# Performance work log

Hardware: AMD Instinct MI355X
Metric: run time of the kernel (lower is better)

## Reference

```python
import jax, jax.numpy as jnp
import numpy as np

DIM = 1024
NUM_HEADS = 16
SCALE = DIM ** (-0.5)  # NOTE: source scales by full dim, not head_dim


def setup_inputs() -> dict:
    key = jax.random.key(0)
    ks = jax.random.split(key, 10)
    B, N, C = 2, 2048, DIM
    s = 0.02
    return {
        "x": jax.random.normal(ks[0], (B, N, C), dtype=jnp.float32),
        "queries": jax.random.normal(ks[1], (B, N, C), dtype=jnp.float32),
        "wq": jax.random.normal(ks[2], (C, C), dtype=jnp.float32) * s,
        "bq": jnp.zeros((C,), dtype=jnp.float32),
        "wk": jax.random.normal(ks[3], (C, C), dtype=jnp.float32) * s,
        "bk": jnp.zeros((C,), dtype=jnp.float32),
        "wv": jax.random.normal(ks[4], (C, C), dtype=jnp.float32) * s,
        "bv": jnp.zeros((C,), dtype=jnp.float32),
        "wo": jax.random.normal(ks[5], (C, C), dtype=jnp.float32) * s,
        "bo": jnp.zeros((C,), dtype=jnp.float32),
    }


def reference(x, queries, wq, bq, wk, bk, wv, bv, wo, bo):
    B, N, C = queries.shape
    H = NUM_HEADS
    D = C // H
    # torch Linear: y = x @ W.T + b  (W is [out, in])
    q = (queries @ wq.T + bq).reshape(B, N, H, D).transpose(0, 2, 1, 3)  # [B,H,N,D]
    k = (x @ wk.T + bk).reshape(B, N, H, D).transpose(0, 2, 1, 3)
    v = (x @ wv.T + bv).reshape(B, N, H, D).transpose(0, 2, 1, 3)
    attn = jnp.einsum("bhqd,bhkd->bhqk", q, k) * SCALE  # full-dim scale per source
    attn = jax.nn.softmax(attn, axis=-1)
    out = jnp.einsum("bhqk,bhkd->bhqd", attn, v)  # [B,H,N,D]
    out = out.transpose(0, 2, 1, 3).reshape(B, N, C)
    return out @ wo.T + bo
```

## Files before the change

### kernel.cpp

```cpp
#include <hip/hip_runtime.h>
#include <hip/hip_bf16.h>

typedef __attribute__((ext_vector_type(8))) short bf16x8;
typedef __attribute__((ext_vector_type(4))) float f32x4;
typedef unsigned short u16;
typedef unsigned int u32;

#define MFMA16(a,b,c) __builtin_amdgcn_mfma_f32_16x16x32_bf16((a),(b),(c),0,0,0)

#if defined(__has_builtin) && __has_builtin(__builtin_amdgcn_exp2f)
#define EXP2(x) __builtin_amdgcn_exp2f(x)
#else
#define EXP2(x) exp2f(x)
#endif

#define QSCALE 0.045084220027780106f

__device__ __forceinline__ u16 f2bf(float f) {
  union { float f; unsigned int u; } v; v.f = f;
  unsigned int r = v.u + 0x7FFFu + ((v.u >> 16) & 1u);
  return (u16)(r >> 16);
}

__device__ __forceinline__ u32 pkbf(float a, float b) {
  union { __hip_bfloat162 h; u32 u; } cv;
  cv.h = __float22bfloat162_rn(make_float2(a, b));
  return cv.u;
}

__device__ __forceinline__ void gld16(const void* g, void* l) {
  __builtin_amdgcn_global_load_lds(
      (__attribute__((address_space(1))) void*)(g),
      (__attribute__((address_space(3))) void*)(l), 16, 0, 0);
}

__global__ __launch_bounds__(256) void cast_all(
    const float* __restrict__ x, const float* __restrict__ qu,
    const float* __restrict__ wq, const float* __restrict__ wk,
    const float* __restrict__ wv, const float* __restrict__ wo,
    u16* __restrict__ xb, u16* __restrict__ qub,
    u16* __restrict__ wqb, u16* __restrict__ wkb,
    u16* __restrict__ wvb, u16* __restrict__ wob)
{
  int i = blockIdx.x * 256 + threadIdx.x;
  const float4* src; u16* dst; int off;
  if (i < 1048576)      { src = (const float4*)qu; dst = qub; off = i; }
  else if (i < 2097152) { src = (const float4*)x;  dst = xb;  off = i - 1048576; }
  else if (i < 2359296) { src = (const float4*)wq; dst = wqb; off = i - 2097152; }
  else if (i < 2621440) { src = (const float4*)wk; dst = wkb; off = i - 2359296; }
  else if (i < 2883584) { src = (const float4*)wv; dst = wvb; off = i - 2621440; }
  else                  { src = (const float4*)wo; dst = wob; off = i - 2883584; }
  float4 v = src[off];
  ushort4 r; r.x = f2bf(v.x); r.y = f2bf(v.y); r.z = f2bf(v.z); r.w = f2bf(v.w);
  ((ushort4*)dst)[off] = r;
}

__global__ __launch_bounds__(256) void gemm_qkv(
    const u16* __restrict__ qub, const u16* __restrict__ xb,
    const u16* __restrict__ wqb, const u16* __restrict__ wkb, const u16* __restrict__ wvb,
    const float* __restrict__ bq, const float* __restrict__ bk, const float* __restrict__ bv,
    u16* __restrict__ qhd, u16* __restrict__ khd, u16* __restrict__ vtd)
{
  __shared__ u16 As[128 * 64];
  __shared__ u16 Bs[128 * 64];
  int tid = threadIdx.x, w = tid >> 6, lane = tid & 63;
  int c = lane & 15, quad = lane >> 4;
  int bm = blockIdx.x, bn = blockIdx.y, z = blockIdx.z;
  int wm = w >> 1, wn = w & 1;
  const u16* A = (z == 0) ? qub : xb;
  const u16* W = (z == 0) ? wqb : (z == 1) ? wkb : wvb;
  f32x4 acc[4][4] = {};
  for (int k0 = 0; k0 < 1024; k0 += 64) {
#pragma unroll
    for (int i = 0; i < 4; i++) {
      int seg = i * 256 + w * 64 + lane;
      int row = seg >> 3, pseg = seg & 7;
      int lseg = pseg ^ (row & 7);
      gld16(A + (size_t)(bm * 128 + row) * 1024 + k0 + lseg * 8,
            &As[(i * 256 + w * 64) * 8]);
      gld16(W + (size_t)(bn * 128 + row) * 1024 + k0 + lseg * 8,
            &Bs[(i * 256 + w * 64) * 8]);
    }
    __syncthreads();
#pragma unroll
    for (int ks = 0; ks < 2; ks++) {
      bf16x8 af[4], bfr[4];
#pragma unroll
      for (int mt = 0; mt < 4; mt++) {
        int row = wm * 64 + mt * 16 + c;
        int cseg = (ks * 4 + quad) ^ (row & 7);
        af[mt] = *(const bf16x8*)&As[(row * 8 + cseg) * 8];
      }
#pragma unroll
      for (int nt = 0; nt < 4; nt++) {
        int row = wn * 64 + nt * 16 + c;
        int cseg = (ks * 4 + quad) ^ (row & 7);
        bfr[nt] = *(const bf16x8*)&Bs[(row * 8 + cseg) * 8];
      }
      if (z < 2) {
#pragma unroll
        for (int ct = 0; ct < 4; ct++)
#pragma unroll
          for (int tt = 0; tt < 4; tt++)
            acc[ct][tt] = MFMA16(bfr[ct], af[tt], acc[ct][tt]);
      } else {
#pragma unroll
        for (int mt = 0; mt < 4; mt++)
#pragma unroll
          for (int nt = 0; nt < 4; nt++)
            acc[mt][nt] = MFMA16(af[mt], bfr[nt], acc[mt][nt]);
      }
    }
    __syncthreads();
  }
  if (z < 2) {
    const float* bias = (z == 0) ? bq : bk;
    u16* dst = (z == 0) ? qhd : khd;
    float sc = (z == 0) ? QSCALE : 1.0f;
    float4 bbs[4];
#pragma unroll
    for (int ct = 0; ct < 4; ct++) {
      float4 b4 = *(const float4*)&bias[bn * 128 + wn * 64 + ct * 16 + quad * 4];
      bbs[ct].x = b4.x * sc; bbs[ct].y = b4.y * sc;
      bbs[ct].z = b4.z * sc; bbs[ct].w = b4.w * sc;
    }
#pragma unroll
    for (int ct = 0; ct < 4; ct++) {
      int ch = bn * 128 + wn * 64 + ct * 16 + quad * 4;
      int h = ch >> 6, d0 = ch & 63;
#pragma unroll
      for (int tt = 0; tt < 4; tt++) {
        int tok = bm * 128 + wm * 64 + tt * 16 + c;
        int b = tok >> 11, n = tok & 2047;
        float v0 = fmaf(acc[ct][tt][0], sc, bbs[ct].x);
        float v1 = fmaf(acc[ct][tt][1], sc, bbs[ct].y);
        float v2 = fmaf(acc[ct][tt][2], sc, bbs[ct].z);
        float v3 = fmaf(acc[ct][tt][3], sc, bbs[ct].w);
        uint2 pk; pk.x = pkbf(v0, v1); pk.y = pkbf(v2, v3);
        *(uint2*)&dst[((size_t)(b * 16 + h) * 2048 + n) * 64 + d0] = pk;
      }
    }
  } else {
    float bval[4];
#pragma unroll
    for (int nt = 0; nt < 4; nt++)
      bval[nt] = bv[bn * 128 + wn * 64 + nt * 16 + c];
#pragma unroll
    for (int mt = 0; mt < 4; mt++) {
      int tokl = (mt & 2) * 16 + quad * 8 + (mt & 1) * 4;
      int tok = bm * 128 + wm * 64 + tokl;
      int b = tok >> 11, np = tok & 2047;
#pragma unroll
      for (int nt = 0; nt < 4; nt++) {
        int ch = bn * 128 + wn * 64 + nt * 16 + c;
        int h = ch >> 6, d = ch & 63;
        float v0 = acc[mt][nt][0] + bval[nt];
        float v1 = acc[mt][nt][1] + bval[nt];
        float v2 = acc[mt][nt][2] + bval[nt];
        float v3 = acc[mt][nt][3] + bval[nt];
        uint2 pk; pk.x = pkbf(v0, v1); pk.y = pkbf(v2, v3);
        *(uint2*)&vtd[((size_t)(b * 16 + h) * 64 + d) * 2048 + np] = pk;
      }
    }
  }
}

__global__ __launch_bounds__(128) void attn(
    const u16* __restrict__ qh, const u16* __restrict__ kh,
    const u16* __restrict__ vt, u16* __restrict__ ot)
{
  __shared__ u16 Kbuf[2][64 * 64];
  __shared__ u16 Vbuf[2][64 * 64];
  int tid = threadIdx.x, w = tid >> 6, lane = tid & 63;
  int c = lane & 15, quad = lane >> 4;
  int bh = blockIdx.x, qt = blockIdx.y;
  const u16* qp = qh + ((size_t)bh * 2048 + qt * 64 + w * 32) * 64;

  bf16x8 Qf[2][2];
#pragma unroll
  for (int qt2 = 0; qt2 < 2; qt2++)
#pragma unroll
    for (int ks = 0; ks < 2; ks++)
      Qf[qt2][ks] = *(const bf16x8*)(qp + (size_t)(qt2 * 16 + c) * 64 + ks * 32 + quad * 8);

  int off0 = c * 64 + ((quad) ^ (c & 7)) * 8;
  int off1 = c * 64 + ((4 + quad) ^ (c & 7)) * 8;

  int sr = lane >> 3;
  int row0 = w * 8 + sr;
  int sls = (lane & 7) ^ (sr & 7);
  const u16* kg = kh + (size_t)bh * 2048 * 64 + row0 * 64 + sls * 8;
  const u16* vg = vt + (size_t)bh * 64 * 2048 + row0 * 2048 + sls * 8;

#define STAGE(B)                                                                \
  {                                                                             \
    gld16(kg,          &Kbuf[B][(w * 64) * 8]);                                 \
    gld16(kg + 1024,   &Kbuf[B][(128 + w * 64) * 8]);                           \
    gld16(kg + 2048,   &Kbuf[B][(256 + w * 64) * 8]);                           \
    gld16(kg + 3072,   &Kbuf[B][(384 + w * 64) * 8]);                           \
    gld16(vg,          &Vbuf[B][(w * 64) * 8]);                                 \
    gld16(vg + 32768,  &Vbuf[B][(128 + w * 64) * 8]);                           \
    gld16(vg + 65536,  &Vbuf[B][(256 + w * 64) * 8]);                           \
    gld16(vg + 98304,  &Vbuf[B][(384 + w * 64) * 8]);                           \
    kg += 4096; vg += 64;                                                       \
  }

  STAGE(0)
  __syncthreads();

  f32x4 O[2][4] = {};
  f32x4 Lacc[2] = {};
  bf16x8 vone;
#pragma unroll
  for (int j = 0; j < 8; j++) vone[j] = (short)0x3F80;

#define ITER(PH, PREF)                                                          \
  {                                                                             \
    if (PREF) STAGE(PH ^ 1)                                                     \
    const u16* Ks = Kbuf[PH];                                                   \
    const u16* Vs = Vbuf[PH];                                                   \
    bf16x8 Kf[4][2];                                                            \
    _Pragma("unroll") for (int nt = 0; nt < 4; nt++) {                          \
      Kf[nt][0] = *(const bf16x8*)&Ks[off0 + nt * 1024];                        \
      Kf[nt][1] = *(const bf16x8*)&Ks[off1 + nt * 1024];                        \
    }                                                                           \
    f32x4 S[2][4] = {};                                                         \
    _Pragma("unroll") for (int qt2 = 0; qt2 < 2; qt2++)                         \
      _Pragma("unroll") for (int nt = 0; nt < 4; nt++) {                        \
        S[qt2][nt] = MFMA16(Kf[nt][0], Qf[qt2][0], S[qt2][nt]);                 \
        S[qt2][nt] = MFMA16(Kf[nt][1], Qf[qt2][1], S[qt2][nt]);                 \
      }                                                                         \
    bf16x8 pa[2][2];                                                            \
    _Pragma("unroll") for (int qt2 = 0; qt2 < 2; qt2++)                         \
      _Pragma("unroll") for (int i = 0; i < 2; i++) {                           \
        float e0 = EXP2(S[qt2][2 * i][0]), e1 = EXP2(S[qt2][2 * i][1]);         \
        float e2 = EXP2(S[qt2][2 * i][2]), e3 = EXP2(S[qt2][2 * i][3]);         \
        float e4 = EXP2(S[qt2][2 * i + 1][0]), e5 = EXP2(S[qt2][2 * i + 1][1]); \
        float e6 = EXP2(S[qt2][2 * i + 1][2]), e7 = EXP2(S[qt2][2 * i + 1][3]); \
        union { uint4 u; bf16x8 v; } cv;                                        \
        cv.u.x = pkbf(e0, e1); cv.u.y = pkbf(e2, e3);                           \
        cv.u.z = pkbf(e4, e5); cv.u.w = pkbf(e6, e7);                           \
        pa[qt2][i] = cv.v;                                                      \
      }                                                                         \
    Lacc[0] = MFMA16(pa[0][0], vone, Lacc[0]);                                  \
    Lacc[0] = MFMA16(pa[0][1], vone, Lacc[0]);                                  \
    Lacc[1] = MFMA16(pa[1][0], vone, Lacc[1]);                                  \
    Lacc[1] = MFMA16(pa[1][1], vone, Lacc[1]);                                  \
    bf16x8 Vf[4][2];                                                            \
    _Pragma("unroll") for (int dt = 0; dt < 4; dt++) {                          \
      Vf[dt][0] = *(const bf16x8*)&Vs[off0 + dt * 1024];                        \
      Vf[dt][1] = *(const bf16x8*)&Vs[off1 + dt * 1024];                        \
    }                                                                           \
    _Pragma("unroll") for (int qt2 = 0; qt2 < 2; qt2++)                         \
      _Pragma("unroll") for (int dt = 0; dt < 4; dt++) {                        \
        O[qt2][dt] = MFMA16(pa[qt2][0], Vf[dt][0], O[qt2][dt]);                 \
        O[qt2][dt] = MFMA16(pa[qt2][1], Vf[dt][1], O[qt2][dt]);                 \
      }                                                                         \
    __syncthreads();                                                            \
  }

  for (int kt2 = 0; kt2 < 15; kt2++) {
    ITER(0, 1)
    ITER(1, 1)
  }
  ITER(0, 1)
  ITER(1, 0)
#undef ITER
#undef STAGE

  int b_ = bh >> 4, h = bh & 15;
#pragma unroll
  for (int qt2 = 0; qt2 < 2; qt2++) {
    f32x4 linv;
#pragma unroll
    for (int j = 0; j < 4; j++) linv[j] = 1.0f / Lacc[qt2][j];
#pragma unroll
    for (int j = 0; j < 4; j++) {
      int n = qt * 64 + w * 32 + qt2 * 16 + quad * 4 + j;
      u16* op = ot + (((size_t)b_ * 2048 + n) * 16 + h) * 64;
#pragma unroll
      for (int dt = 0; dt < 4; dt++)
        op[dt * 16 + c] = f2bf(O[qt2][dt][j] * linv[j]);
    }
  }
}

__global__ __launch_bounds__(256) void gemm_out(
    const u16* __restrict__ Aot, const u16* __restrict__ wob,
    const float* __restrict__ bo, float* __restrict__ out)
{
  __shared__ u16 As[64 * 64];
  __shared__ u16 Bs[128 * 64];
  int tid = threadIdx.x, w = tid >> 6, lane = tid & 63;
  int bm = blockIdx.x, bn = blockIdx.y;
  int wm = w >> 1, wn = w & 1;
  f32x4 acc[2][4] = {};
  for (int k0 = 0; k0 < 1024; k0 += 64) {
#pragma unroll
    for (int i = 0; i < 2; i++) {
      int seg = i * 256 + tid;
      int row = seg >> 3, pseg = seg & 7;
      int lseg = pseg ^ (row & 7);
      gld16(Aot + (size_t)(bm * 64 + row) * 1024 + k0 + lseg * 8,
            &As[(i * 256 + tid - (tid & 7)) * 8 + (tid & 7) * 8]);
    }
#pragma unroll
    for (int i = 0; i < 4; i++) {
      int seg = i * 256 + tid;
      int row = seg >> 3, pseg = seg & 7;
      int lseg = pseg ^ (row & 7);
      gld16(wob + (size_t)(bn * 128 + row) * 1024 + k0 + lseg * 8,
            &Bs[(i * 256 + tid - (tid & 7)) * 8 + (tid & 7) * 8]);
    }
    __syncthreads();
#pragma unroll
    for (int ks = 0; ks < 2; ks++) {
      bf16x8 af[2], bfr[4];
#pragma unroll
      for (int mt = 0; mt < 2; mt++) {
        int row = wm * 32 + mt * 16 + (lane & 15);
        int cseg = (ks * 4 + (lane >> 4)) ^ (row & 7);
        af[mt] = *(const bf16x8*)&As[(row * 8 + cseg) * 8];
      }
#pragma unroll
      for (int nt = 0; nt < 4; nt++) {
        int row = wn * 64 + nt * 16 + (lane & 15);
        int cseg = (ks * 4 + (lane >> 4)) ^ (row & 7);
        bfr[nt] = *(const bf16x8*)&Bs[(row * 8 + cseg) * 8];
      }
#pragma unroll
      for (int mt = 0; mt < 2; mt++)
#pragma unroll
        for (int nt = 0; nt < 4; nt++)
          acc[mt][nt] = MFMA16(af[mt], bfr[nt], acc[mt][nt]);
    }
    __syncthreads();
  }
#pragma unroll
  for (int nt = 0; nt < 4; nt++) {
    int o = bn * 128 + wn * 64 + nt * 16 + (lane & 15);
    float bval = bo[o];
#pragma unroll
    for (int mt = 0; mt < 2; mt++)
#pragma unroll
      for (int j = 0; j < 4; j++) {
        int m = bm * 64 + wm * 32 + mt * 16 + (lane >> 4) * 4 + j;
        out[(size_t)m * 1024 + o] = acc[mt][nt][j] + bval;
      }
  }
}

extern "C" void kernel_launch(void* const* d_in, const int* in_sizes, int n_in,
                              void* d_out, int out_size, void* d_ws, size_t ws_size,
                              hipStream_t stream)
{
  const float* x  = (const float*)d_in[0];
  const float* qu = (const float*)d_in[1];
  const float* wq = (const float*)d_in[2];
  const float* bq = (const float*)d_in[3];
  const float* wk = (const float*)d_in[4];
  const float* bk = (const float*)d_in[5];
  const float* wv = (const float*)d_in[6];
  const float* bv = (const float*)d_in[7];
  const float* wo = (const float*)d_in[8];
  const float* bo = (const float*)d_in[9];
  float* out = (float*)d_out;
  char* ws = (char*)d_ws;
  u16* xb  = (u16*)(ws + (size_t)0);
  u16* qub = (u16*)(ws + ((size_t)8  << 20));
  u16* wqb = (u16*)(ws + ((size_t)16 << 20));
  u16* wkb = (u16*)(ws + ((size_t)18 << 20));
  u16* wvb = (u16*)(ws + ((size_t)20 << 20));
  u16* wob = (u16*)(ws + ((size_t)22 << 20));
  u16* qhd = (u16*)(ws + ((size_t)24 << 20));
  u16* khd = (u16*)(ws + ((size_t)32 << 20));
  u16* vtd = (u16*)(ws + ((size_t)40 << 20));
  u16* otd = (u16*)(ws + ((size_t)48 << 20));

  cast_all<<<12288, 256, 0, stream>>>(x, qu, wq, wk, wv, wo,
                                      xb, qub, wqb, wkb, wvb, wob);
  gemm_qkv<<<dim3(32, 8, 3), 256, 0, stream>>>(qub, xb, wqb, wkb, wvb,
                                               bq, bk, bv, qhd, khd, vtd);
  attn<<<dim3(32, 32), 128, 0, stream>>>(qhd, khd, vtd, otd);
  gemm_out<<<dim3(64, 8), 256, 0, stream>>>(otd, wob, bo, out);
}
```

Before: 204.2 us.

## Split attention over two KV halves with a separate combine kernel

Attention now launches a second grid dimension so each block handles half of the key sequence with 32-key tiles. Unnormalized partial outputs and row sums go to fp32 workspace, and a new combine kernel adds the halves, normalizes and writes bf16. This doubles the number of blocks for better CU occupancy and latency hiding. The cost is extra global traffic for the fp32 partials, an extra launch, and fewer MFMAs per barrier.

```diff
diff --git a/kernel.cpp b/kernel.cpp
--- a/kernel.cpp
+++ b/kernel.cpp
@@ -167,13 +167,14 @@
 
 __global__ __launch_bounds__(128) void attn(
     const u16* __restrict__ qh, const u16* __restrict__ kh,
-    const u16* __restrict__ vt, u16* __restrict__ ot)
-{
-  __shared__ u16 Kbuf[2][64 * 64];
-  __shared__ u16 Vbuf[2][64 * 64];
+    const u16* __restrict__ vt,
+    float* __restrict__ po0, float* __restrict__ po1, float* __restrict__ pl)
+{
+  __shared__ u16 Kbuf[2][32 * 64];
+  __shared__ u16 Vbuf[2][64 * 32];
   int tid = threadIdx.x, w = tid >> 6, lane = tid & 63;
   int c = lane & 15, quad = lane >> 4;
-  int bh = blockIdx.x, qt = blockIdx.y;
+  int bh = blockIdx.x, qt = blockIdx.y, kv = blockIdx.z;
   const u16* qp = qh + ((size_t)bh * 2048 + qt * 64 + w * 32) * 64;
 
   bf16x8 Qf[2][2];
@@ -183,26 +184,26 @@
     for (int ks = 0; ks < 2; ks++)
       Qf[qt2][ks] = *(const bf16x8*)(qp + (size_t)(qt2 * 16 + c) * 64 + ks * 32 + quad * 8);
 
-  int off0 = c * 64 + ((quad) ^ (c & 7)) * 8;
-  int off1 = c * 64 + ((4 + quad) ^ (c & 7)) * 8;
-
-  int sr = lane >> 3;
-  int row0 = w * 8 + sr;
-  int sls = (lane & 7) ^ (sr & 7);
-  const u16* kg = kh + (size_t)bh * 2048 * 64 + row0 * 64 + sls * 8;
-  const u16* vg = vt + (size_t)bh * 64 * 2048 + row0 * 2048 + sls * 8;
+  int offK0 = c * 64 + ((quad) ^ (c & 7)) * 8;
+  int offK1 = c * 64 + ((4 + quad) ^ (c & 7)) * 8;
+  int offV  = c * 32 + ((quad ^ ((c >> 1) & 3))) * 8;
+
+  int kr = w * 16 + (lane >> 3);
+  const u16* kg = kh + (size_t)bh * 2048 * 64 + kv * 1024 * 64 +
+                  kr * 64 + ((lane & 7) ^ (kr & 7)) * 8;
+  int vr = w * 32 + (lane >> 2);
+  const u16* vg = vt + (size_t)bh * 64 * 2048 + vr * 2048 + kv * 1024 +
+                  ((lane & 3) ^ ((vr >> 1) & 3)) * 8;
+  u16* kd0[2] = {&Kbuf[0][(w * 2) * 512],     &Kbuf[1][(w * 2) * 512]};
+  u16* kd1[2] = {&Kbuf[0][(w * 2 + 1) * 512], &Kbuf[1][(w * 2 + 1) * 512]};
+  u16* vd0[2] = {&Vbuf[0][(w * 2) * 512],     &Vbuf[1][(w * 2) * 512]};
+  u16* vd1[2] = {&Vbuf[0][(w * 2 + 1) * 512], &Vbuf[1][(w * 2 + 1) * 512]};
 
 #define STAGE(B)                                                                \
   {                                                                             \
-    gld16(kg,          &Kbuf[B][(w * 64) * 8]);                                 \
-    gld16(kg + 1024,   &Kbuf[B][(128 + w * 64) * 8]);                           \
-    gld16(kg + 2048,   &Kbuf[B][(256 + w * 64) * 8]);                           \
-    gld16(kg + 3072,   &Kbuf[B][(384 + w * 64) * 8]);                           \
-    gld16(vg,          &Vbuf[B][(w * 64) * 8]);                                 \
-    gld16(vg + 32768,  &Vbuf[B][(128 + w * 64) * 8]);                           \
-    gld16(vg + 65536,  &Vbuf[B][(256 + w * 64) * 8]);                           \
-    gld16(vg + 98304,  &Vbuf[B][(384 + w * 64) * 8]);                           \
-    kg += 4096; vg += 64;                                                       \
+    gld16(kg,         kd0[B]); gld16(kg + 512,       kd1[B]);                   \
+    gld16(vg,         vd0[B]); gld16(vg + 16 * 2048, vd1[B]);                   \
+    kg += 2048; vg += 32;                                                       \
   }
 
   STAGE(0)
@@ -210,6 +211,7 @@
 
   f32x4 O[2][4] = {};
   f32x4 Lacc[2] = {};
+  const f32x4 Zv = {};
   bf16x8 vone;
 #pragma unroll
   for (int j = 0; j < 8; j++) vone[j] = (short)0x3F80;
@@ -219,43 +221,36 @@
     if (PREF) STAGE(PH ^ 1)                                                     \
     const u16* Ks = Kbuf[PH];                                                   \
     const u16* Vs = Vbuf[PH];                                                   \
-    bf16x8 Kf[4][2];                                                            \
-    _Pragma("unroll") for (int nt = 0; nt < 4; nt++) {                          \
-      Kf[nt][0] = *(const bf16x8*)&Ks[off0 + nt * 1024];                        \
-      Kf[nt][1] = *(const bf16x8*)&Ks[off1 + nt * 1024];                        \
+    bf16x8 Kf[2][2];                                                            \
+    _Pragma("unroll") for (int nt = 0; nt < 2; nt++) {                          \
+      Kf[nt][0] = *(const bf16x8*)&Ks[offK0 + nt * 1024];                       \
+      Kf[nt][1] = *(const bf16x8*)&Ks[offK1 + nt * 1024];                       \
     }                                                                           \
-    f32x4 S[2][4] = {};                                                         \
+    f32x4 S[2][2];                                                              \
     _Pragma("unroll") for (int qt2 = 0; qt2 < 2; qt2++)                         \
-      _Pragma("unroll") for (int nt = 0; nt < 4; nt++) {                        \
-        S[qt2][nt] = MFMA16(Kf[nt][0], Qf[qt2][0], S[qt2][nt]);                 \
+      _Pragma("unroll") for (int nt = 0; nt < 2; nt++) {                        \
+        S[qt2][nt] = MFMA16(Kf[nt][0], Qf[qt2][0], Zv);                         \
         S[qt2][nt] = MFMA16(Kf[nt][1], Qf[qt2][1], S[qt2][nt]);                 \
       }                                                                         \
-    bf16x8 pa[2][2];                                                            \
+    bf16x8 pa[2];                                                               \
+    _Pragma("unroll") for (int qt2 = 0; qt2 < 2; qt2++) {                       \
+      float e0 = EXP2(S[qt2][0][0]), e1 = EXP2(S[qt2][0][1]);                   \
+      float e2 = EXP2(S[qt2][0][2]), e3 = EXP2(S[qt2][0][3]);                   \
+      float e4 = EXP2(S[qt2][1][0]), e5 = EXP2(S[qt2][1][1]);                   \
+      float e6 = EXP2(S[qt2][1][2]), e7 = EXP2(S[qt2][1][3]);                   \
+      union { uint4 u; bf16x8 v; } cv;                                          \
+      cv.u.x = pkbf(e0, e1); cv.u.y = pkbf(e2, e3);                             \
+      cv.u.z = pkbf(e4, e5); cv.u.w = pkbf(e6, e7);                             \
+      pa[qt2] = cv.v;                                                           \
+    }                                                                           \
+    Lacc[0] = MFMA16(pa[0], vone, Lacc[0]);                                     \
+    Lacc[1] = MFMA16(pa[1], vone, Lacc[1]);                                     \
+    bf16x8 Vf[4];                                                               \
+    _Pragma("unroll") for (int dt = 0; dt < 4; dt++)                            \
+      Vf[dt] = *(const bf16x8*)&Vs[offV + dt * 512];                            \
     _Pragma("unroll") for (int qt2 = 0; qt2 < 2; qt2++)                         \
-      _Pragma("unroll") for (int i = 0; i < 2; i++) {                           \
-        float e0 = EXP2(S[qt2][2 * i][0]), e1 = EXP2(S[qt2][2 * i][1]);         \
-        float e2 = EXP2(S[qt2][2 * i][2]), e3 = EXP2(S[qt2][2 * i][3]);         \
-        float e4 = EXP2(S[qt2][2 * i + 1][0]), e5 = EXP2(S[qt2][2 * i + 1][1]); \
-        float e6 = EXP2(S[qt2][2 * i + 1][2]), e7 = EXP2(S[qt2][2 * i + 1][3]); \
-        union { uint4 u; bf16x8 v; } cv;                                        \
-        cv.u.x = pkbf(e0, e1); cv.u.y = pkbf(e2, e3);                           \
-        cv.u.z = pkbf(e4, e5); cv.u.w = pkbf(e6, e7);                           \
-        pa[qt2][i] = cv.v;                                                      \
-      }                                                                         \
-    Lacc[0] = MFMA16(pa[0][0], vone, Lacc[0]);                                  \
-    Lacc[0] = MFMA16(pa[0][1], vone, Lacc[0]);                                  \
-    Lacc[1] = MFMA16(pa[1][0], vone, Lacc[1]);                                  \
-    Lacc[1] = MFMA16(pa[1][1], vone, Lacc[1]);                                  \
-    bf16x8 Vf[4][2];                                                            \
-    _Pragma("unroll") for (int dt = 0; dt < 4; dt++) {                          \
-      Vf[dt][0] = *(const bf16x8*)&Vs[off0 + dt * 1024];                        \
-      Vf[dt][1] = *(const bf16x8*)&Vs[off1 + dt * 1024];                        \
-    }                                                                           \
-    _Pragma("unroll") for (int qt2 = 0; qt2 < 2; qt2++)                         \
-      _Pragma("unroll") for (int dt = 0; dt < 4; dt++) {                        \
-        O[qt2][dt] = MFMA16(pa[qt2][0], Vf[dt][0], O[qt2][dt]);                 \
-        O[qt2][dt] = MFMA16(pa[qt2][1], Vf[dt][1], O[qt2][dt]);                 \
-      }                                                                         \
+      _Pragma("unroll") for (int dt = 0; dt < 4; dt++)                          \
+        O[qt2][dt] = MFMA16(pa[qt2], Vf[dt], O[qt2][dt]);                       \
     __syncthreads();                                                            \
   }
 
@@ -268,21 +263,37 @@
 #undef ITER
 #undef STAGE
 
+  float* pob = (kv ? po1 : po0) +
+               (((size_t)bh * 2048) + qt * 64 + w * 32) * 64;
+  float* plb = pl + (size_t)kv * 65536 + bh * 2048 + qt * 64 + w * 32;
+#pragma unroll
+  for (int qt2 = 0; qt2 < 2; qt2++)
+#pragma unroll
+    for (int j = 0; j < 4; j++) {
+      int nl = qt2 * 16 + quad * 4 + j;
+#pragma unroll
+      for (int dt = 0; dt < 4; dt++)
+        pob[nl * 64 + dt * 16 + c] = O[qt2][dt][j];
+      if (c == 0) plb[nl] = Lacc[qt2][j];
+    }
+}
+
+__global__ __launch_bounds__(256) void combine(
+    const float* __restrict__ po0, const float* __restrict__ po1,
+    const float* __restrict__ pl, u16* __restrict__ ot)
+{
+  int t = blockIdx.x * 256 + threadIdx.x;
+  int dq = t & 15, n = (t >> 4) & 2047, bh = t >> 15;
+  size_t i0 = (((size_t)bh * 2048) + n) * 64 + dq * 4;
+  f32x4 a = *(const f32x4*)(po0 + i0);
+  f32x4 b = *(const f32x4*)(po1 + i0);
+  float l = pl[bh * 2048 + n] + pl[65536 + bh * 2048 + n];
+  float inv = 1.0f / l;
   int b_ = bh >> 4, h = bh & 15;
-#pragma unroll
-  for (int qt2 = 0; qt2 < 2; qt2++) {
-    f32x4 linv;
-#pragma unroll
-    for (int j = 0; j < 4; j++) linv[j] = 1.0f / Lacc[qt2][j];
-#pragma unroll
-    for (int j = 0; j < 4; j++) {
-      int n = qt * 64 + w * 32 + qt2 * 16 + quad * 4 + j;
-      u16* op = ot + (((size_t)b_ * 2048 + n) * 16 + h) * 64;
-#pragma unroll
-      for (int dt = 0; dt < 4; dt++)
-        op[dt * 16 + c] = f2bf(O[qt2][dt][j] * linv[j]);
-    }
-  }
+  uint2 pk;
+  pk.x = pkbf((a[0] + b[0]) * inv, (a[1] + b[1]) * inv);
+  pk.y = pkbf((a[2] + b[2]) * inv, (a[3] + b[3]) * inv);
+  *(uint2*)(ot + (((size_t)b_ * 2048 + n) * 16 + h) * 64 + dq * 4) = pk;
 }
 
 __global__ __launch_bounds__(256) void gemm_out(
@@ -376,11 +387,15 @@
   u16* khd = (u16*)(ws + ((size_t)32 << 20));
   u16* vtd = (u16*)(ws + ((size_t)40 << 20));
   u16* otd = (u16*)(ws + ((size_t)48 << 20));
+  float* po0 = (float*)(ws + (size_t)0);
+  float* po1 = (float*)(ws + ((size_t)56 << 20));
+  float* pl  = (float*)(ws + ((size_t)72 << 20));
 
   cast_all<<<12288, 256, 0, stream>>>(x, qu, wq, wk, wv, wo,
                                       xb, qub, wqb, wkb, wvb, wob);
   gemm_qkv<<<dim3(32, 8, 3), 256, 0, stream>>>(qub, xb, wqb, wkb, wvb,
                                                bq, bk, bv, qhd, khd, vtd);
-  attn<<<dim3(32, 32), 128, 0, stream>>>(qhd, khd, vtd, otd);
+  attn<<<dim3(32, 32, 2), 128, 0, stream>>>(qhd, khd, vtd, po0, po1, pl);
+  combine<<<4096, 256, 0, stream>>>(po0, po1, pl, otd);
   gemm_out<<<dim3(64, 8), 256, 0, stream>>>(otd, wob, bo, out);
 }
```

Result: slower. 222.5 us (+9.0%).
